# Optimization experiments

Hardware: AMD Instinct MI355X
Metric: run time of the kernel (lower is better)

The kernel has to match this reference:

```python
import jax, jax.numpy as jnp
import numpy as np

NUM_HEADS = 12

def setup_inputs() -> dict:
    key = jax.random.key(0)
    ks = jax.random.split(key, 9)
    B, N, C = 4, 1024, 768
    hd = C // NUM_HEADS  # 64
    return {
        "x": jax.random.normal(ks[0], (B, N, C), dtype=jnp.float32),
        "prev_attn": jax.random.uniform(ks[1], (B, NUM_HEADS, N, N), dtype=jnp.float32) / N,
        "qkv_w": jax.random.normal(ks[2], (3 * C, C), dtype=jnp.float32) * 0.02,
        "proj_w": jax.random.normal(ks[3], (C, C), dtype=jnp.float32) * 0.02,
        "proj_b": jax.random.normal(ks[4], (C,), dtype=jnp.float32) * 0.02,
        "bp_w1": jax.random.normal(ks[5], (hd // 2, 2 * hd), dtype=jnp.float32) * 0.02,
        "bp_b1": jax.random.normal(ks[6], (hd // 2,), dtype=jnp.float32) * 0.02,
        "bp_w2": jax.random.normal(ks[7], (3, hd // 2), dtype=jnp.float32) * 0.02,
        "bp_b2": jax.random.normal(ks[8], (3,), dtype=jnp.float32) * 0.02,
    }

def reference(x, prev_attn, qkv_w, proj_w, proj_b, bp_w1, bp_b1, bp_w2, bp_b2):
    B, N, C = x.shape
    H = NUM_HEADS
    hd = C // H
    scale = hd ** -0.5
    # qkv projection: [B,N,3C] -> [3,B,H,N,hd]
    qkv = (x @ qkv_w.T).reshape(B, N, 3, H, hd).transpose(2, 0, 3, 1, 4)
    q, k, v = qkv[0], qkv[1], qkv[2]
    # scaled dot-product scores [B,H,N,N]
    attn_logits = jnp.einsum('bhnd,bhmd->bhnm', q, k) * scale
    cur_attn = jax.nn.softmax(attn_logits, axis=-1)
    # per-(b,h,n) bias MLP on concat(q,k): [B,H,N,2*hd] -> [B,H,N,3]
    qk = jnp.concatenate((q, k), axis=-1)
    h1 = jax.nn.relu(jnp.einsum('bhnd,od->bhno', qk, bp_w1) + bp_b1)
    bias = jnp.abs(jnp.einsum('bhno,po->bhnp', h1, bp_w2) + bp_b2)  # [B,H,N,3]
    # blend current attention, previous attention, and uniform term
    attn = (cur_attn * (1.0 + bias[..., 0:1])
            + prev_attn * bias[..., 1:2]
            - bias[..., 2:3] / N)
    out = jnp.einsum('bhnm,bhmd->bhnd', attn, v)  # [B,H,N,hd]
    out = out.transpose(0, 2, 1, 3).reshape(B, N, C)
    out = out @ proj_w.T + proj_b
    return (out, cur_attn)
```

## Files before the change

kernel.cpp:

```cpp
#include <hip/hip_runtime.h>

typedef __bf16 bf16_t;
typedef __bf16 bf16x8 __attribute__((ext_vector_type(8)));
typedef __bf16 bf16x4 __attribute__((ext_vector_type(4)));
typedef float f32x4 __attribute__((ext_vector_type(4)));

static constexpr int Bb = 4, Hh = 12, Nn = 1024, Cc = 768, HD = 64;
static constexpr int OUT0 = Bb * Nn * Cc;

#define GLD16(gp, lp)                                                       \
  __builtin_amdgcn_global_load_lds(                                         \
      (const __attribute__((address_space(1))) unsigned int*)(gp),          \
      (__attribute__((address_space(3))) unsigned int*)(lp), 16, 0, 0)

__global__ __launch_bounds__(256) void convert_all(
    const float* __restrict__ x, const float* __restrict__ qw, const float* __restrict__ pw,
    bf16_t* __restrict__ xb, bf16_t* __restrict__ qwb, bf16_t* __restrict__ pwb) {
  const int NX = (Bb * Nn * Cc) / 4;
  const int NQ = (3 * Cc * Cc) / 4;
  int i = blockIdx.x * 256 + threadIdx.x;
  const float4* src;
  bf16_t* dst;
  int off;
  if (i < NX) { src = (const float4*)x; dst = xb; off = i; }
  else if (i < NX + NQ) { src = (const float4*)qw; dst = qwb; off = i - NX; }
  else { src = (const float4*)pw; dst = pwb; off = i - NX - NQ; }
  float4 v = src[off];
  bf16x4 o;
  o[0] = (bf16_t)v.x; o[1] = (bf16_t)v.y; o[2] = (bf16_t)v.z; o[3] = (bf16_t)v.w;
  *(bf16x4*)(dst + (size_t)off * 4) = o;
}

__global__ __launch_bounds__(256) void gemm_qkv(
    const bf16_t* __restrict__ A, const bf16_t* __restrict__ Bm,
    bf16_t* __restrict__ q_bf, bf16_t* __restrict__ k_bf, bf16_t* __restrict__ vT_bf) {
  __shared__ bf16_t As[128 * 32];
  __shared__ bf16_t Bs[128 * 32];
  const int tid = threadIdx.x;
  const int lane = tid & 63;
  const int w = tid >> 6;
  const int wr = w >> 1, wc = w & 1;
  const int g = lane >> 4, r = lane & 15;
  const int m0 = (blockIdx.x / 18) << 7;
  const int n0 = (blockIdx.x % 18) << 7;

  const f32x4 fz = {0.f, 0.f, 0.f, 0.f};
  f32x4 acc[4][4];
#pragma unroll
  for (int i = 0; i < 4; i++)
#pragma unroll
    for (int j = 0; j < 4; j++) acc[i][j] = fz;

  for (int k0 = 0; k0 < 768; k0 += 32) {
#pragma unroll
    for (int c = 0; c < 2; c++) {
      int row = w * 32 + c * 16 + (lane >> 2);
      int kof = (lane & 3) << 3;
      GLD16(&A[(size_t)(m0 + row) * 768 + k0 + kof], (char*)As + w * 2048 + c * 1024);
      GLD16(&Bm[(size_t)(n0 + row) * 768 + k0 + kof], (char*)Bs + w * 2048 + c * 1024);
    }
    __syncthreads();
    bf16x8 af[4], bfv[4];
#pragma unroll
    for (int i = 0; i < 4; i++) af[i] = *(const bf16x8*)&As[(wr * 64 + i * 16 + r) * 32 + g * 8];
#pragma unroll
    for (int j = 0; j < 4; j++) bfv[j] = *(const bf16x8*)&Bs[(wc * 64 + j * 16 + r) * 32 + g * 8];
#pragma unroll
    for (int i = 0; i < 4; i++)
#pragma unroll
      for (int j = 0; j < 4; j++)
        acc[i][j] = __builtin_amdgcn_mfma_f32_16x16x32_bf16(af[i], bfv[j], acc[i][j], 0, 0, 0);
    __syncthreads();
  }

#pragma unroll
  for (int i = 0; i < 4; i++) {
#pragma unroll
    for (int j = 0; j < 4; j++) {
      int c = n0 + wc * 64 + j * 16 + r;
#pragma unroll
      for (int e = 0; e < 4; e++) {
        int mrow = m0 + wr * 64 + i * 16 + g * 4 + e;
        float val = acc[i][j][e];
        int which = c / 768;
        int cc = c - which * 768;
        int h = cc >> 6, d = cc & 63;
        int b = mrow >> 10, n = mrow & 1023;
        size_t bh = (size_t)(b * Hh + h);
        if (which == 0)      q_bf[(bh * Nn + n) * HD + d] = (bf16_t)val;
        else if (which == 1) k_bf[(bh * Nn + n) * HD + d] = (bf16_t)val;
        else                 vT_bf[(bh * HD + d) * Nn + n] = (bf16_t)val;
      }
    }
  }
}

template <int MODE>
__global__ __launch_bounds__(256) void gemm_bt(
    const bf16_t* __restrict__ A, const bf16_t* __restrict__ Bm, int N, int K,
    float* __restrict__ outF, const float* __restrict__ bias) {
  __shared__ bf16_t As[128 * 40];
  __shared__ bf16_t Bs[128 * 40];
  const int tid = threadIdx.x;
  const int lane = tid & 63;
  const int w = tid >> 6;
  const int wr = w >> 1, wc = w & 1;
  const int g = lane >> 4, r = lane & 15;
  const int ntiles = N >> 7;
  const int m0 = (blockIdx.x / ntiles) << 7;
  const int n0 = (blockIdx.x % ntiles) << 7;

  const f32x4 fz = {0.f, 0.f, 0.f, 0.f};
  f32x4 acc[4][4];
#pragma unroll
  for (int i = 0; i < 4; i++)
#pragma unroll
    for (int j = 0; j < 4; j++) acc[i][j] = fz;

  for (int k0 = 0; k0 < K; k0 += 32) {
#pragma unroll
    for (int p = 0; p < 2; p++) {
      int idx = tid + (p << 8);
      int row = idx >> 2;
      int kof = (idx & 3) << 3;
      *(bf16x8*)&As[row * 40 + kof] = *(const bf16x8*)&A[(size_t)(m0 + row) * K + k0 + kof];
      *(bf16x8*)&Bs[row * 40 + kof] = *(const bf16x8*)&Bm[(size_t)(n0 + row) * K + k0 + kof];
    }
    __syncthreads();
    bf16x8 af[4], bfv[4];
#pragma unroll
    for (int i = 0; i < 4; i++) af[i] = *(const bf16x8*)&As[(wr * 64 + i * 16 + r) * 40 + g * 8];
#pragma unroll
    for (int j = 0; j < 4; j++) bfv[j] = *(const bf16x8*)&Bs[(wc * 64 + j * 16 + r) * 40 + g * 8];
#pragma unroll
    for (int i = 0; i < 4; i++)
#pragma unroll
      for (int j = 0; j < 4; j++)
        acc[i][j] = __builtin_amdgcn_mfma_f32_16x16x32_bf16(af[i], bfv[j], acc[i][j], 0, 0, 0);
    __syncthreads();
  }

#pragma unroll
  for (int i = 0; i < 4; i++) {
#pragma unroll
    for (int j = 0; j < 4; j++) {
      int c = n0 + wc * 64 + j * 16 + r;
#pragma unroll
      for (int e = 0; e < 4; e++) {
        int mrow = m0 + wr * 64 + i * 16 + g * 4 + e;
        outF[(size_t)mrow * N + c] = acc[i][j][e] + bias[c];
      }
    }
  }
}

__global__ __launch_bounds__(256) void bias_mlp(
    const bf16_t* __restrict__ qb, const bf16_t* __restrict__ kb,
    const float* __restrict__ w1, const float* __restrict__ b1,
    const float* __restrict__ w2, const float* __restrict__ b2,
    float* __restrict__ bias4) {
  __shared__ float w1s[32 * 130];
  __shared__ float qks[8][128];
  __shared__ float h1s[8][32];
  const int t = threadIdx.x;
#pragma unroll
  for (int p = 0; p < 16; p++) {
    int idx = p * 256 + t;
    w1s[(idx >> 7) * 130 + (idx & 127)] = w1[idx];
  }
  const int rl = t >> 5, u = t & 31;
  const int rowg = blockIdx.x * 8 + rl;
  {
    int i4 = u * 4;
    const bf16_t* src = (i4 < 64) ? (qb + (size_t)rowg * HD + i4)
                                  : (kb + (size_t)rowg * HD + (i4 - 64));
    bf16x4 vv = *(const bf16x4*)src;
#pragma unroll
    for (int z = 0; z < 4; z++) qks[rl][i4 + z] = (float)vv[z];
  }
  __syncthreads();
  float accv = b1[u];
#pragma unroll 16
  for (int i2 = 0; i2 < 64; i2++) {
    float2 wv = *(const float2*)&w1s[u * 130 + i2 * 2];
    float2 qv = *(const float2*)&qks[rl][i2 * 2];
    accv += wv.x * qv.x + wv.y * qv.y;
  }
  h1s[rl][u] = fmaxf(accv, 0.f);
  __syncthreads();
  if (u < 4) {
    float outv = 0.f;
    if (u < 3) {
      float s = b2[u];
#pragma unroll
      for (int j = 0; j < 32; j++) s += w2[u * 32 + j] * h1s[rl][j];
      float v = fabsf(s);
      outv = (u == 0) ? (1.f + v) : ((u == 1) ? v : -v * (1.f / (float)Nn));
    }
    bias4[(size_t)rowg * 4 + u] = outv;
  }
}

__global__ __launch_bounds__(256, 2) void attn_fused(
    const bf16_t* __restrict__ qb, const bf16_t* __restrict__ kb,
    const bf16_t* __restrict__ vT, const float* __restrict__ prev,
    const float* __restrict__ bias4, float* __restrict__ cur,
    bf16_t* __restrict__ oh) {
  __shared__ char Plb[32 * 2048];
  __shared__ float redmax[32][4];
  __shared__ float redsum[32][4];
  const int bid = blockIdx.x;
  const int tile = (bid & 7) * 192 + (bid >> 3);
  const int bh = tile >> 5, mt = tile & 31;
  const int tid = threadIdx.x;
  const int lane = tid & 63, w = tid >> 6;
  const int g = lane >> 4, r = lane & 15;
  const int row0 = mt << 5;
  const int cbase = w << 8;

  const bf16_t* qp = qb + ((size_t)bh * Nn + row0) * HD;
  const bf16_t* kp = kb + (size_t)bh * Nn * HD;
  bf16x8 q00 = *(const bf16x8*)&qp[r * HD + g * 8];
  bf16x8 q01 = *(const bf16x8*)&qp[r * HD + g * 8 + 32];
  bf16x8 q10 = *(const bf16x8*)&qp[(16 + r) * HD + g * 8];
  bf16x8 q11 = *(const bf16x8*)&qp[(16 + r) * HD + g * 8 + 32];
  bf16x8 qa0, qa1, qb0, qb1;
#pragma unroll
  for (int j = 0; j < 8; j++) {
    qa0[j] = (bf16_t)((float)q00[j] * 0.125f);
    qa1[j] = (bf16_t)((float)q01[j] * 0.125f);
    qb0[j] = (bf16_t)((float)q10[j] * 0.125f);
    qb1[j] = (bf16_t)((float)q11[j] * 0.125f);
  }
  const f32x4 fz = {0.f, 0.f, 0.f, 0.f};
  f32x4 acc0[16], acc1[16];
#pragma unroll
  for (int t = 0; t < 16; t++) {
    int col = cbase + (t << 4) + r;
    bf16x8 kf0 = *(const bf16x8*)&kp[(size_t)col * HD + g * 8];
    bf16x8 kf1 = *(const bf16x8*)&kp[(size_t)col * HD + g * 8 + 32];
    f32x4 z0 = __builtin_amdgcn_mfma_f32_16x16x32_bf16(kf0, qa0, fz, 0, 0, 0);
    acc0[t] = __builtin_amdgcn_mfma_f32_16x16x32_bf16(kf1, qa1, z0, 0, 0, 0);
    f32x4 z1 = __builtin_amdgcn_mfma_f32_16x16x32_bf16(kf0, qb0, fz, 0, 0, 0);
    acc1[t] = __builtin_amdgcn_mfma_f32_16x16x32_bf16(kf1, qb1, z1, 0, 0, 0);
  }

  float mj0 = -3.0e38f, mj1 = -3.0e38f;
#pragma unroll
  for (int t = 0; t < 16; t++)
#pragma unroll
    for (int e = 0; e < 4; e++) {
      mj0 = fmaxf(mj0, acc0[t][e]);
      mj1 = fmaxf(mj1, acc1[t][e]);
    }
  mj0 = fmaxf(mj0, __shfl_xor(mj0, 16, 64));
  mj0 = fmaxf(mj0, __shfl_xor(mj0, 32, 64));
  mj1 = fmaxf(mj1, __shfl_xor(mj1, 16, 64));
  mj1 = fmaxf(mj1, __shfl_xor(mj1, 32, 64));
  if (lane < 16) {
    redmax[lane][w] = mj0;
    redmax[16 + lane][w] = mj1;
  }
  __syncthreads();
  float rm0, rm1;
  {
    float v0 = fmaxf(redmax[r][0], redmax[r][1]);
    rm0 = fmaxf(v0, fmaxf(redmax[r][2], redmax[r][3]));
    float v1 = fmaxf(redmax[16 + r][0], redmax[16 + r][1]);
    rm1 = fmaxf(v1, fmaxf(redmax[16 + r][2], redmax[16 + r][3]));
  }
  float sj0 = 0.f, sj1 = 0.f;
  bf16x4 p0[16], p1[16];
#pragma unroll
  for (int t = 0; t < 16; t++) {
    float a0 = __expf(acc0[t][0] - rm0), a1 = __expf(acc0[t][1] - rm0);
    float a2 = __expf(acc0[t][2] - rm0), a3 = __expf(acc0[t][3] - rm0);
    sj0 += (a0 + a1) + (a2 + a3);
    p0[t][0] = (bf16_t)a0; p0[t][1] = (bf16_t)a1;
    p0[t][2] = (bf16_t)a2; p0[t][3] = (bf16_t)a3;
    float b0v = __expf(acc1[t][0] - rm1), b1v = __expf(acc1[t][1] - rm1);
    float b2v = __expf(acc1[t][2] - rm1), b3v = __expf(acc1[t][3] - rm1);
    sj1 += (b0v + b1v) + (b2v + b3v);
    p1[t][0] = (bf16_t)b0v; p1[t][1] = (bf16_t)b1v;
    p1[t][2] = (bf16_t)b2v; p1[t][3] = (bf16_t)b3v;
  }
  sj0 += __shfl_xor(sj0, 16, 64);
  sj0 += __shfl_xor(sj0, 32, 64);
  sj1 += __shfl_xor(sj1, 16, 64);
  sj1 += __shfl_xor(sj1, 32, 64);
  if (lane < 16) {
    redsum[lane][w] = sj0;
    redsum[16 + lane][w] = sj1;
  }
  __syncthreads();
  const float inv0 =
      1.f / (redsum[r][0] + redsum[r][1] + redsum[r][2] + redsum[r][3]);
  const float inv1 =
      1.f / (redsum[16 + r][0] + redsum[16 + r][1] + redsum[16 + r][2] + redsum[16 + r][3]);

  const float4 bv0 = *(const float4*)&bias4[((size_t)bh * 1024 + row0 + r) * 4];
  const float4 bv1 = *(const float4*)&bias4[((size_t)bh * 1024 + row0 + 16 + r) * 4];
  {
    const float* ppr = prev + (size_t)bh * Nn * Nn + (size_t)(row0 + r) * Nn + cbase + (g << 2);
    float* cp = cur + (size_t)bh * Nn * Nn + (size_t)(row0 + r) * Nn + cbase + (g << 2);
#pragma unroll
    for (int t = 0; t < 16; t++) {
      float4 pvv = *(const float4*)&ppr[t << 4];
      float4 p;
      p.x = (float)p0[t][0] * inv0;
      p.y = (float)p0[t][1] * inv0;
      p.z = (float)p0[t][2] * inv0;
      p.w = (float)p0[t][3] * inv0;
      *(float4*)&cp[t << 4] = p;
      bf16x4 nb;
      nb[0] = (bf16_t)(bv0.x * p.x + bv0.y * pvv.x + bv0.z);
      nb[1] = (bf16_t)(bv0.x * p.y + bv0.y * pvv.y + bv0.z);
      nb[2] = (bf16_t)(bv0.x * p.z + bv0.y * pvv.z + bv0.z);
      nb[3] = (bf16_t)(bv0.x * p.w + bv0.y * pvv.w + bv0.z);
      int col = cbase + (t << 4) + (g << 2);
      int off = (r * 2048 + col * 2) ^ ((r & 7) << 4);
      *(bf16x4*)(Plb + off) = nb;
    }
  }
  {
    const float* ppr = prev + (size_t)bh * Nn * Nn + (size_t)(row0 + 16 + r) * Nn + cbase + (g << 2);
    float* cp = cur + (size_t)bh * Nn * Nn + (size_t)(row0 + 16 + r) * Nn + cbase + (g << 2);
#pragma unroll
    for (int t = 0; t < 16; t++) {
      float4 pvv = *(const float4*)&ppr[t << 4];
      float4 p;
      p.x = (float)p1[t][0] * inv1;
      p.y = (float)p1[t][1] * inv1;
      p.z = (float)p1[t][2] * inv1;
      p.w = (float)p1[t][3] * inv1;
      *(float4*)&cp[t << 4] = p;
      bf16x4 nb;
      nb[0] = (bf16_t)(bv1.x * p.x + bv1.y * pvv.x + bv1.z);
      nb[1] = (bf16_t)(bv1.x * p.y + bv1.y * pvv.y + bv1.z);
      nb[2] = (bf16_t)(bv1.x * p.z + bv1.y * pvv.z + bv1.z);
      nb[3] = (bf16_t)(bv1.x * p.w + bv1.y * pvv.w + bv1.z);
      int col = cbase + (t << 4) + (g << 2);
      int off = ((16 + r) * 2048 + col * 2) ^ ((r & 7) << 4);
      *(bf16x4*)(Plb + off) = nb;
    }
  }
  __syncthreads();

  const bf16_t* vrow = vT + (size_t)bh * HD * Nn + (size_t)((w << 4) + r) * Nn;
  f32x4 o0q0 = fz, o0q1 = fz, o0q2 = fz, o0q3 = fz;
  f32x4 o1q0 = fz, o1q1 = fz, o1q2 = fz, o1q3 = fz;
#pragma unroll
  for (int ks = 0; ks < 8; ks++) {
    int kA = ks << 5;
#pragma unroll
    for (int q = 0; q < 4; q++) {
      int k0 = (q << 8) + kA;
      bf16x8 vb = *(const bf16x8*)&vrow[k0 + g * 8];
      bf16x8 pa0 = *(const bf16x8*)(Plb + ((r * 2048 + (k0 + g * 8) * 2) ^ ((r & 7) << 4)));
      bf16x8 pa1 = *(const bf16x8*)(Plb + (((16 + r) * 2048 + (k0 + g * 8) * 2) ^ ((r & 7) << 4)));
      if (q == 0) {
        o0q0 = __builtin_amdgcn_mfma_f32_16x16x32_bf16(pa0, vb, o0q0, 0, 0, 0);
        o1q0 = __builtin_amdgcn_mfma_f32_16x16x32_bf16(pa1, vb, o1q0, 0, 0, 0);
      } else if (q == 1) {
        o0q1 = __builtin_amdgcn_mfma_f32_16x16x32_bf16(pa0, vb, o0q1, 0, 0, 0);
        o1q1 = __builtin_amdgcn_mfma_f32_16x16x32_bf16(pa1, vb, o1q1, 0, 0, 0);
      } else if (q == 2) {
        o0q2 = __builtin_amdgcn_mfma_f32_16x16x32_bf16(pa0, vb, o0q2, 0, 0, 0);
        o1q2 = __builtin_amdgcn_mfma_f32_16x16x32_bf16(pa1, vb, o1q2, 0, 0, 0);
      } else {
        o0q3 = __builtin_amdgcn_mfma_f32_16x16x32_bf16(pa0, vb, o0q3, 0, 0, 0);
        o1q3 = __builtin_amdgcn_mfma_f32_16x16x32_bf16(pa1, vb, o1q3, 0, 0, 0);
      }
    }
  }
  f32x4 os0 = (o0q0 + o0q1) + (o0q2 + o0q3);
  f32x4 os1 = (o1q0 + o1q1) + (o1q2 + o1q3);
  const int b = bh / Hh, h = bh % Hh;
#pragma unroll
  for (int e = 0; e < 4; e++) {
    int nrow = row0 + g * 4 + e;
    oh[((size_t)(b * Nn + nrow)) * Cc + h * HD + (w << 4) + r] = (bf16_t)os0[e];
    oh[((size_t)(b * Nn + nrow + 16)) * Cc + h * HD + (w << 4) + r] = (bf16_t)os1[e];
  }
}

extern "C" void kernel_launch(void* const* d_in, const int* in_sizes, int n_in,
                              void* d_out, int out_size, void* d_ws, size_t ws_size,
                              hipStream_t stream) {
  const float* x      = (const float*)d_in[0];
  const float* prev   = (const float*)d_in[1];
  const float* qkv_w  = (const float*)d_in[2];
  const float* proj_w = (const float*)d_in[3];
  const float* proj_b = (const float*)d_in[4];
  const float* bp_w1  = (const float*)d_in[5];
  const float* bp_b1  = (const float*)d_in[6];
  const float* bp_w2  = (const float*)d_in[7];
  const float* bp_w2b = (const float*)d_in[8];

  float* out0 = (float*)d_out;
  float* cur  = out0 + OUT0;

  char* ws = (char*)d_ws;
  bf16_t* xb    = (bf16_t*)(ws + 0);
  bf16_t* qwb   = (bf16_t*)(ws + 6291456);
  bf16_t* pwb   = (bf16_t*)(ws + 9830400);
  bf16_t* qbf   = (bf16_t*)(ws + 11010048);
  bf16_t* kbf   = (bf16_t*)(ws + 17301504);
  bf16_t* vtb   = (bf16_t*)(ws + 23592960);
  float*  bias4 = (float*)(ws + 29884416);
  bf16_t* ohb   = (bf16_t*)(ws + 30670848);
  if (ws_size < 36962304) return;

  convert_all<<<5376, 256, 0, stream>>>(x, qkv_w, proj_w, xb, qwb, pwb);
  gemm_qkv<<<32 * 18, 256, 0, stream>>>(xb, qwb, qbf, kbf, vtb);
  bias_mlp<<<49152 / 8, 256, 0, stream>>>(qbf, kbf, bp_w1, bp_b1, bp_w2, bp_w2b, bias4);
  attn_fused<<<1536, 256, 0, stream>>>(qbf, kbf, vtb, prev, bias4, cur, ohb);
  gemm_bt<1><<<(4096 / 128) * (768 / 128), 256, 0, stream>>>(
      ohb, pwb, 768, 768, out0, proj_b);
}
```

Measured before the change: 226.0 us.

## Split attention tile across eight waves with split-K PV reduction

The fused attention block grows from 256 to 512 threads, so each wave handles 128 score columns instead of 256, which halves the per-thread accumulator and probability register arrays. The PV product is split across two wave halves along the key dimension, and the partial sums are combined through a new shared buffer plus an extra barrier. The goal is higher occupancy and more latency hiding for the memory-heavy prev/cur traffic. The cost is more cross-wave reduction work, one more synchronisation, and a larger LDS footprint per block, which could limit how many blocks fit per CU.

```diff
diff --git a/kernel.cpp b/kernel.cpp
--- a/kernel.cpp
+++ b/kernel.cpp
@@ -201,14 +201,15 @@
   }
 }
 
-__global__ __launch_bounds__(256, 2) void attn_fused(
+__global__ __launch_bounds__(512, 4) void attn_fused(
     const bf16_t* __restrict__ qb, const bf16_t* __restrict__ kb,
     const bf16_t* __restrict__ vT, const float* __restrict__ prev,
     const float* __restrict__ bias4, float* __restrict__ cur,
     bf16_t* __restrict__ oh) {
   __shared__ char Plb[32 * 2048];
-  __shared__ float redmax[32][4];
-  __shared__ float redsum[32][4];
+  __shared__ float redmax[32][8];
+  __shared__ float redsum[32][8];
+  __shared__ f32x4 part[2][4][64];
   const int bid = blockIdx.x;
   const int tile = (bid & 7) * 192 + (bid >> 3);
   const int bh = tile >> 5, mt = tile & 31;
@@ -216,7 +217,7 @@
   const int lane = tid & 63, w = tid >> 6;
   const int g = lane >> 4, r = lane & 15;
   const int row0 = mt << 5;
-  const int cbase = w << 8;
+  const int cbase = w << 7;
 
   const bf16_t* qp = qb + ((size_t)bh * Nn + row0) * HD;
   const bf16_t* kp = kb + (size_t)bh * Nn * HD;
@@ -233,9 +234,9 @@
     qb1[j] = (bf16_t)((float)q11[j] * 0.125f);
   }
   const f32x4 fz = {0.f, 0.f, 0.f, 0.f};
-  f32x4 acc0[16], acc1[16];
-#pragma unroll
-  for (int t = 0; t < 16; t++) {
+  f32x4 acc0[8], acc1[8];
+#pragma unroll
+  for (int t = 0; t < 8; t++) {
     int col = cbase + (t << 4) + r;
     bf16x8 kf0 = *(const bf16x8*)&kp[(size_t)col * HD + g * 8];
     bf16x8 kf1 = *(const bf16x8*)&kp[(size_t)col * HD + g * 8 + 32];
@@ -247,7 +248,7 @@
 
   float mj0 = -3.0e38f, mj1 = -3.0e38f;
 #pragma unroll
-  for (int t = 0; t < 16; t++)
+  for (int t = 0; t < 8; t++)
 #pragma unroll
     for (int e = 0; e < 4; e++) {
       mj0 = fmaxf(mj0, acc0[t][e]);
@@ -262,17 +263,16 @@
     redmax[16 + lane][w] = mj1;
   }
   __syncthreads();
-  float rm0, rm1;
-  {
-    float v0 = fmaxf(redmax[r][0], redmax[r][1]);
-    rm0 = fmaxf(v0, fmaxf(redmax[r][2], redmax[r][3]));
-    float v1 = fmaxf(redmax[16 + r][0], redmax[16 + r][1]);
-    rm1 = fmaxf(v1, fmaxf(redmax[16 + r][2], redmax[16 + r][3]));
+  float rm0 = redmax[r][0], rm1 = redmax[16 + r][0];
+#pragma unroll
+  for (int q = 1; q < 8; q++) {
+    rm0 = fmaxf(rm0, redmax[r][q]);
+    rm1 = fmaxf(rm1, redmax[16 + r][q]);
   }
   float sj0 = 0.f, sj1 = 0.f;
-  bf16x4 p0[16], p1[16];
-#pragma unroll
-  for (int t = 0; t < 16; t++) {
+  bf16x4 p0[8], p1[8];
+#pragma unroll
+  for (int t = 0; t < 8; t++) {
     float a0 = __expf(acc0[t][0] - rm0), a1 = __expf(acc0[t][1] - rm0);
     float a2 = __expf(acc0[t][2] - rm0), a3 = __expf(acc0[t][3] - rm0);
     sj0 += (a0 + a1) + (a2 + a3);
@@ -293,10 +293,13 @@
     redsum[16 + lane][w] = sj1;
   }
   __syncthreads();
-  const float inv0 =
-      1.f / (redsum[r][0] + redsum[r][1] + redsum[r][2] + redsum[r][3]);
-  const float inv1 =
-      1.f / (redsum[16 + r][0] + redsum[16 + r][1] + redsum[16 + r][2] + redsum[16 + r][3]);
+  float s0 = redsum[r][0], s1 = redsum[16 + r][0];
+#pragma unroll
+  for (int q = 1; q < 8; q++) {
+    s0 += redsum[r][q];
+    s1 += redsum[16 + r][q];
+  }
+  const float inv0 = 1.f / s0, inv1 = 1.f / s1;
 
   const float4 bv0 = *(const float4*)&bias4[((size_t)bh * 1024 + row0 + r) * 4];
   const float4 bv1 = *(const float4*)&bias4[((size_t)bh * 1024 + row0 + 16 + r) * 4];
@@ -304,7 +307,7 @@
     const float* ppr = prev + (size_t)bh * Nn * Nn + (size_t)(row0 + r) * Nn + cbase + (g << 2);
     float* cp = cur + (size_t)bh * Nn * Nn + (size_t)(row0 + r) * Nn + cbase + (g << 2);
 #pragma unroll
-    for (int t = 0; t < 16; t++) {
+    for (int t = 0; t < 8; t++) {
       float4 pvv = *(const float4*)&ppr[t << 4];
       float4 p;
       p.x = (float)p0[t][0] * inv0;
@@ -326,7 +329,7 @@
     const float* ppr = prev + (size_t)bh * Nn * Nn + (size_t)(row0 + 16 + r) * Nn + cbase + (g << 2);
     float* cp = cur + (size_t)bh * Nn * Nn + (size_t)(row0 + 16 + r) * Nn + cbase + (g << 2);
 #pragma unroll
-    for (int t = 0; t < 16; t++) {
+    for (int t = 0; t < 8; t++) {
       float4 pvv = *(const float4*)&ppr[t << 4];
       float4 p;
       p.x = (float)p1[t][0] * inv1;
@@ -346,41 +349,40 @@
   }
   __syncthreads();
 
-  const bf16_t* vrow = vT + (size_t)bh * HD * Nn + (size_t)((w << 4) + r) * Nn;
-  f32x4 o0q0 = fz, o0q1 = fz, o0q2 = fz, o0q3 = fz;
-  f32x4 o1q0 = fz, o1q1 = fz, o1q2 = fz, o1q3 = fz;
-#pragma unroll
-  for (int ks = 0; ks < 8; ks++) {
-    int kA = ks << 5;
-#pragma unroll
-    for (int q = 0; q < 4; q++) {
-      int k0 = (q << 8) + kA;
-      bf16x8 vb = *(const bf16x8*)&vrow[k0 + g * 8];
-      bf16x8 pa0 = *(const bf16x8*)(Plb + ((r * 2048 + (k0 + g * 8) * 2) ^ ((r & 7) << 4)));
-      bf16x8 pa1 = *(const bf16x8*)(Plb + (((16 + r) * 2048 + (k0 + g * 8) * 2) ^ ((r & 7) << 4)));
-      if (q == 0) {
-        o0q0 = __builtin_amdgcn_mfma_f32_16x16x32_bf16(pa0, vb, o0q0, 0, 0, 0);
-        o1q0 = __builtin_amdgcn_mfma_f32_16x16x32_bf16(pa1, vb, o1q0, 0, 0, 0);
-      } else if (q == 1) {
-        o0q1 = __builtin_amdgcn_mfma_f32_16x16x32_bf16(pa0, vb, o0q1, 0, 0, 0);
-        o1q1 = __builtin_amdgcn_mfma_f32_16x16x32_bf16(pa1, vb, o1q1, 0, 0, 0);
-      } else if (q == 2) {
-        o0q2 = __builtin_amdgcn_mfma_f32_16x16x32_bf16(pa0, vb, o0q2, 0, 0, 0);
-        o1q2 = __builtin_amdgcn_mfma_f32_16x16x32_bf16(pa1, vb, o1q2, 0, 0, 0);
-      } else {
-        o0q3 = __builtin_amdgcn_mfma_f32_16x16x32_bf16(pa0, vb, o0q3, 0, 0, 0);
-        o1q3 = __builtin_amdgcn_mfma_f32_16x16x32_bf16(pa1, vb, o1q3, 0, 0, 0);
-      }
-    }
-  }
-  f32x4 os0 = (o0q0 + o0q1) + (o0q2 + o0q3);
-  f32x4 os1 = (o1q0 + o1q1) + (o1q2 + o1q3);
-  const int b = bh / Hh, h = bh % Hh;
-#pragma unroll
-  for (int e = 0; e < 4; e++) {
-    int nrow = row0 + g * 4 + e;
-    oh[((size_t)(b * Nn + nrow)) * Cc + h * HD + (w << 4) + r] = (bf16_t)os0[e];
-    oh[((size_t)(b * Nn + nrow + 16)) * Cc + h * HD + (w << 4) + r] = (bf16_t)os1[e];
+  const int dg = w & 3, kh = w >> 2;
+  const bf16_t* vrow = vT + (size_t)bh * HD * Nn + (size_t)((dg << 4) + r) * Nn;
+  f32x4 o0a = fz, o0b = fz, o1a = fz, o1b = fz;
+#pragma unroll
+  for (int ks = 0; ks < 16; ks++) {
+    int k0 = (kh << 9) + (ks << 5);
+    bf16x8 vb = *(const bf16x8*)&vrow[k0 + g * 8];
+    bf16x8 pa0 = *(const bf16x8*)(Plb + ((r * 2048 + (k0 + g * 8) * 2) ^ ((r & 7) << 4)));
+    bf16x8 pa1 = *(const bf16x8*)(Plb + (((16 + r) * 2048 + (k0 + g * 8) * 2) ^ ((r & 7) << 4)));
+    if (ks & 1) {
+      o0b = __builtin_amdgcn_mfma_f32_16x16x32_bf16(pa0, vb, o0b, 0, 0, 0);
+      o1b = __builtin_amdgcn_mfma_f32_16x16x32_bf16(pa1, vb, o1b, 0, 0, 0);
+    } else {
+      o0a = __builtin_amdgcn_mfma_f32_16x16x32_bf16(pa0, vb, o0a, 0, 0, 0);
+      o1a = __builtin_amdgcn_mfma_f32_16x16x32_bf16(pa1, vb, o1a, 0, 0, 0);
+    }
+  }
+  f32x4 os0 = o0a + o0b;
+  f32x4 os1 = o1a + o1b;
+  if (kh == 1) {
+    part[0][dg][lane] = os0;
+    part[1][dg][lane] = os1;
+  }
+  __syncthreads();
+  if (kh == 0) {
+    f32x4 t0 = os0 + part[0][dg][lane];
+    f32x4 t1 = os1 + part[1][dg][lane];
+    const int b = bh / Hh, h = bh % Hh;
+#pragma unroll
+    for (int e = 0; e < 4; e++) {
+      int nrow = row0 + g * 4 + e;
+      oh[((size_t)(b * Nn + nrow)) * Cc + h * HD + (dg << 4) + r] = (bf16_t)t0[e];
+      oh[((size_t)(b * Nn + nrow + 16)) * Cc + h * HD + (dg << 4) + r] = (bf16_t)t1[e];
+    }
   }
 }
 
@@ -414,7 +416,7 @@
   convert_all<<<5376, 256, 0, stream>>>(x, qkv_w, proj_w, xb, qwb, pwb);
   gemm_qkv<<<32 * 18, 256, 0, stream>>>(xb, qwb, qbf, kbf, vtb);
   bias_mlp<<<49152 / 8, 256, 0, stream>>>(qbf, kbf, bp_w1, bp_b1, bp_w2, bp_w2b, bias4);
-  attn_fused<<<1536, 256, 0, stream>>>(qbf, kbf, vtb, prev, bias4, cur, ohb);
+  attn_fused<<<1536, 512, 0, stream>>>(qbf, kbf, vtb, prev, bias4, cur, ohb);
   gemm_bt<1><<<(4096 / 128) * (768 / 128), 256, 0, stream>>>(
       ohb, pwb, 768, 768, out0, proj_b);
 }
```

Result: slower. 233.9 us (+3.5%).
